# Kernel tuning notes

Hardware: AMD Instinct MI355X
Metric: run time of the kernel (lower is better)

Reference implementation:

```python
import jax, jax.numpy as jnp
import numpy as np

NUM_HEADS = 12
HEAD_DIM = 64  # dim=768 // 12
SCALE = HEAD_DIM ** (-0.5)  # NOTE: original divides q by this -> multiplies by sqrt(head_dim)


def setup_inputs() -> dict:
    key = jax.random.key(0)
    k1, k2, k3 = jax.random.split(key, 3)
    B, N, C = 1, 4096, 768
    x = jax.random.normal(k1, (B, N, C), dtype=jnp.float32)
    qkv_w = jax.random.normal(k2, (3 * C, C), dtype=jnp.float32) * 0.01
    qkv_b = jnp.zeros((3 * C,), dtype=jnp.float32)
    proj_w = jax.random.normal(k3, (C, C), dtype=jnp.float32) * 0.01
    proj_b = jnp.zeros((C,), dtype=jnp.float32)
    return {"x": x, "qkv_w": qkv_w, "qkv_b": qkv_b, "proj_w": proj_w, "proj_b": proj_b}


def reference(x, qkv_w, qkv_b, proj_w, proj_b):
    B, N, C = x.shape
    H, D = NUM_HEADS, HEAD_DIM
    # qkv projection: [B,N,3C]
    qkv = x @ qkv_w.T + qkv_b
    qkv = qkv.reshape(B, N, 3, H, D).transpose(2, 0, 3, 1, 4)  # [3,B,H,N,D]
    q, k, v = qkv[0], qkv[1], qkv[2]
    # Faithful quirk: q / scale with scale = D**-0.5 => logits scaled by sqrt(D)
    attn = jnp.einsum('bhnd,bhmd->bhnm', q / SCALE, k)  # [B,H,N,N]
    attn = jax.nn.softmax(attn, axis=-1)
    # dropout omitted (eval mode / deterministic reference)
    out = jnp.einsum('bhnm,bhmd->bhnd', attn, v)  # [B,H,N,D]
    out = out.transpose(0, 2, 1, 3).reshape(B, N, C)
    out = out @ proj_w.T + proj_b
    return out
```

## Files before the change

kernel.cpp:

```cpp
#include <hip/hip_runtime.h>


typedef short bf16x8 __attribute__((ext_vector_type(8)));
typedef float f32x4 __attribute__((ext_vector_type(4)));
typedef unsigned short u16;
typedef unsigned int u32;

__device__ __forceinline__ u16 f2bf(float f) {
  u32 u = __float_as_uint(f);
  u = (u + 0x7fffu + ((u >> 16) & 1u)) >> 16;
  return (u16)u;
}

__device__ __forceinline__ u32 packbf(float a, float b) {
  u32 ua = __float_as_uint(a), ub = __float_as_uint(b);
  ua += 0x7fffu + ((ua >> 16) & 1u);
  ub += 0x7fffu + ((ub >> 16) & 1u);
  return __builtin_amdgcn_perm(ub, ua, 0x07060302);
}

__device__ __forceinline__ void gload16(const void* g, void* l) {
  __builtin_amdgcn_global_load_lds(
      (const __attribute__((address_space(1))) unsigned int*)g,
      (__attribute__((address_space(3))) unsigned int*)l, 16, 0, 0);
}

__global__ void cast3(const float* __restrict__ a, int na4,
                      const float* __restrict__ b, int nb4,
                      const float* __restrict__ c, int nc4,
                      u16* __restrict__ oa, u16* __restrict__ obp, u16* __restrict__ oc) {
  int i = blockIdx.x * blockDim.x + threadIdx.x;
  const float* src;
  u16* dst;
  int j = i;
  if (i < na4) { src = a; dst = oa; }
  else if (i < na4 + nb4) { src = b; dst = obp; j = i - na4; }
  else if (i < na4 + nb4 + nc4) { src = c; dst = oc; j = i - na4 - nb4; }
  else return;
  float4 v = ((const float4*)src)[j];
  ushort4 o;
  o.x = f2bf(v.x); o.y = f2bf(v.y); o.z = f2bf(v.z); o.w = f2bf(v.w);
  ((ushort4*)dst)[j] = o;
}

template <int MODE>
__global__ __launch_bounds__(256, 2) void gemm_bt(
    const u16* __restrict__ A, const u16* __restrict__ B,
    const float* __restrict__ bias,
    u16* __restrict__ qb, u16* __restrict__ kbuf, u16* __restrict__ vb,
    float* __restrict__ outp, int K, int N) {
  __shared__ __align__(16) u16 As[128 * 32];
  __shared__ __align__(16) u16 Bs[128 * 32];
  const int tid = threadIdx.x, lane = tid & 63, w = tid >> 6;
  const int wr = w >> 1, wc = w & 1, quad = lane >> 4, l15 = lane & 15;
  const int m0 = blockIdx.y * 128, n0 = blockIdx.x * 128;

  f32x4 acc[4][4];
#pragma unroll
  for (int i = 0; i < 4; ++i)
#pragma unroll
    for (int j = 0; j < 4; ++j) acc[i][j] = (f32x4){0.f, 0.f, 0.f, 0.f};

  for (int k0 = 0; k0 < K; k0 += 32) {
    __syncthreads();
#pragma unroll
    for (int i = 0; i < 2; ++i) {
      int chunk = i * 256 + w * 64 + lane;
      int row = chunk >> 2, kc = chunk & 3;
      gload16(A + (size_t)(m0 + row) * K + k0 + kc * 8, (char*)As + chunk * 16);
      gload16(B + (size_t)(n0 + row) * K + k0 + kc * 8, (char*)Bs + chunk * 16);
    }
    __syncthreads();
    bf16x8 af[4], bfr[4];
#pragma unroll
    for (int mi = 0; mi < 4; ++mi)
      af[mi] = *(const bf16x8*)&As[(wr * 64 + mi * 16 + l15) * 32 + quad * 8];
#pragma unroll
    for (int ni = 0; ni < 4; ++ni)
      bfr[ni] = *(const bf16x8*)&Bs[(wc * 64 + ni * 16 + l15) * 32 + quad * 8];
#pragma unroll
    for (int mi = 0; mi < 4; ++mi)
#pragma unroll
      for (int ni = 0; ni < 4; ++ni)
        acc[mi][ni] = __builtin_amdgcn_mfma_f32_16x16x32_bf16(af[mi], bfr[ni], acc[mi][ni], 0, 0, 0);
  }

#pragma unroll
  for (int mi = 0; mi < 4; ++mi) {
    int row = m0 + wr * 64 + mi * 16 + quad * 4;
#pragma unroll
    for (int ni = 0; ni < 4; ++ni) {
      int col = n0 + wc * 64 + ni * 16 + l15;
      float bv = bias[col];
      if (MODE == 0) {
        int t = col / 768;
        int rem = col - t * 768;
        int hh = rem >> 6, d = rem & 63;
        if (t == 2) {
          u16* dst = vb + (size_t)hh * 64 * 4096 + (size_t)d * 4096 + row;
          ushort4 pk;
          pk.x = f2bf(acc[mi][ni][0] + bv);
          pk.y = f2bf(acc[mi][ni][1] + bv);
          pk.z = f2bf(acc[mi][ni][2] + bv);
          pk.w = f2bf(acc[mi][ni][3] + bv);
          *(ushort4*)dst = pk;
        } else {
          u16* dst = (t == 0 ? qb : kbuf) + (size_t)hh * 4096 * 64 + d;
          float sc = (t == 0) ? 11.541560327111707f : 1.f;
#pragma unroll
          for (int r = 0; r < 4; ++r)
            dst[(size_t)(row + r) * 64] = f2bf((acc[mi][ni][r] + bv) * sc);
        }
      } else {
#pragma unroll
        for (int r = 0; r < 4; ++r)
          outp[(size_t)(row + r) * N + col] = acc[mi][ni][r] + bv;
      }
    }
  }
}

__global__ __launch_bounds__(256, 3) void flash_attn(
    const u16* __restrict__ qb, const u16* __restrict__ kb,
    const u16* __restrict__ vtg, u16* __restrict__ ob) {
  constexpr int PLS = 72;
  __shared__ __align__(16) u16 Ks[2][64 * 64];
  __shared__ __align__(16) u16 Vs[2][64 * 64];
  __shared__ __align__(16) u16 pl[4][16 * PLS];

  const int b = blockIdx.x;
  const int g = (b & 7) * 96 + (b >> 3);
  const int h = g >> 6;
  const int q0 = (g & 63) * 64;

  const int tid = threadIdx.x, lane = tid & 63, w = tid >> 6;
  const int quad = lane >> 4, l15 = lane & 15;
  const u16* qh = qb + (size_t)h * 4096 * 64;
  const u16* kh = kb + (size_t)h * 4096 * 64;
  const u16* vh = vtg + (size_t)h * 64 * 4096;
  u16* mypl = &pl[w][0];
  const int sw = l15 & 7;
  const int u0 = (quad ^ sw) * 8;
  const int u1 = ((quad + 4) ^ sw) * 8;

  int c0 = w * 64 + lane, c1 = 256 + w * 64 + lane;
  int r0s = c0 >> 3, j0s = ((c0 & 7) ^ (r0s & 7)) * 8;
  int r1s = c1 >> 3, j1s = ((c1 & 7) ^ (r1s & 7)) * 8;

  bf16x8 qf[2];
#pragma unroll
  for (int c = 0; c < 2; ++c)
    qf[c] = *(const bf16x8*)&qh[(size_t)(q0 + w * 16 + l15) * 64 + c * 32 + quad * 8];

  f32x4 oacc[4];
#pragma unroll
  for (int dt = 0; dt < 4; ++dt) oacc[dt] = (f32x4){0.f, 0.f, 0.f, 0.f};
  float lsum = 0.f;

  gload16(kh + (size_t)r0s * 64 + j0s, (char*)&Ks[0][0] + c0 * 16);
  gload16(kh + (size_t)r1s * 64 + j1s, (char*)&Ks[0][0] + c1 * 16);
  gload16(vh + (size_t)r0s * 4096 + j0s, (char*)&Vs[0][0] + c0 * 16);
  gload16(vh + (size_t)r1s * 4096 + j1s, (char*)&Vs[0][0] + c1 * 16);

  for (int t = 0; t < 64; ++t) {
    const int buf = t & 1;
    __syncthreads();
    if (t < 63) {
      int kt1 = (t + 1) * 64;
      gload16(kh + (size_t)(kt1 + r0s) * 64 + j0s, (char*)&Ks[buf ^ 1][0] + c0 * 16);
      gload16(kh + (size_t)(kt1 + r1s) * 64 + j1s, (char*)&Ks[buf ^ 1][0] + c1 * 16);
      gload16(vh + (size_t)r0s * 4096 + kt1 + j0s, (char*)&Vs[buf ^ 1][0] + c0 * 16);
      gload16(vh + (size_t)r1s * 4096 + kt1 + j1s, (char*)&Vs[buf ^ 1][0] + c1 * 16);
    }

    f32x4 st[4];
#pragma unroll
    for (int nt = 0; nt < 4; ++nt) {
      const u16* kp = &Ks[buf][(nt * 16 + l15) * 64];
      bf16x8 kf0 = *(const bf16x8*)(kp + u0);
      bf16x8 kf1 = *(const bf16x8*)(kp + u1);
      f32x4 z = (f32x4){0.f, 0.f, 0.f, 0.f};
      z = __builtin_amdgcn_mfma_f32_16x16x32_bf16(kf0, qf[0], z, 0, 0, 0);
      st[nt] = __builtin_amdgcn_mfma_f32_16x16x32_bf16(kf1, qf[1], z, 0, 0, 0);
    }

    bf16x8 vf0[4], vf1[4];
#pragma unroll
    for (int dt = 0; dt < 4; ++dt) {
      const u16* vp = &Vs[buf][(dt * 16 + l15) * 64];
      vf0[dt] = *(const bf16x8*)(vp + u0);
      vf1[dt] = *(const bf16x8*)(vp + u1);
    }

    float ls = 0.f;
#pragma unroll
    for (int nt = 0; nt < 4; ++nt) {
      float p0 = __builtin_amdgcn_exp2f(st[nt][0]);
      float p1 = __builtin_amdgcn_exp2f(st[nt][1]);
      float p2 = __builtin_amdgcn_exp2f(st[nt][2]);
      float p3 = __builtin_amdgcn_exp2f(st[nt][3]);
      ls += (p0 + p1) + (p2 + p3);
      uint2 pk;
      pk.x = packbf(p0, p1);
      pk.y = packbf(p2, p3);
      *(uint2*)&mypl[l15 * PLS + nt * 16 + quad * 4] = pk;
    }
    lsum += ls;

    bf16x8 pf0 = *(const bf16x8*)&mypl[l15 * PLS + quad * 8];
    bf16x8 pf1 = *(const bf16x8*)&mypl[l15 * PLS + 32 + quad * 8];
#pragma unroll
    for (int dt = 0; dt < 4; ++dt) {
      oacc[dt] = __builtin_amdgcn_mfma_f32_16x16x32_bf16(pf0, vf0[dt], oacc[dt], 0, 0, 0);
      oacc[dt] = __builtin_amdgcn_mfma_f32_16x16x32_bf16(pf1, vf1[dt], oacc[dt], 0, 0, 0);
    }
  }

  lsum += __shfl_xor(lsum, 16);
  lsum += __shfl_xor(lsum, 32);
  float linv = 1.f / lsum;
  float r0 = __shfl(linv, quad * 4 + 0);
  float r1 = __shfl(linv, quad * 4 + 1);
  float r2 = __shfl(linv, quad * 4 + 2);
  float r3 = __shfl(linv, quad * 4 + 3);
#pragma unroll
  for (int dt = 0; dt < 4; ++dt) {
    int d = dt * 16 + l15;
    int row = q0 + w * 16 + quad * 4;
    u16* op = ob + (size_t)row * 768 + h * 64 + d;
    op[0]       = f2bf(oacc[dt][0] * r0);
    op[768]     = f2bf(oacc[dt][1] * r1);
    op[2 * 768] = f2bf(oacc[dt][2] * r2);
    op[3 * 768] = f2bf(oacc[dt][3] * r3);
  }
}

extern "C" void kernel_launch(void* const* d_in, const int* in_sizes, int n_in,
                              void* d_out, int out_size, void* d_ws, size_t ws_size,
                              hipStream_t stream) {
  const float* x      = (const float*)d_in[0];
  const float* qkv_w  = (const float*)d_in[1];
  const float* qkv_b  = (const float*)d_in[2];
  const float* proj_w = (const float*)d_in[3];
  const float* proj_b = (const float*)d_in[4];
  float* out = (float*)d_out;

  const int N = 4096, C = 768, H = 12, D = 64, C3 = 2304;
  char* ws = (char*)d_ws;
  size_t off = 0;
  u16* xb    = (u16*)(ws + off); off += (size_t)N * C * 2;
  u16* wqkv  = (u16*)(ws + off); off += (size_t)C3 * C * 2;
  u16* wproj = (u16*)(ws + off); off += (size_t)C * C * 2;
  u16* qbuf  = (u16*)(ws + off); off += (size_t)H * N * D * 2;
  u16* kbuf  = (u16*)(ws + off); off += (size_t)H * N * D * 2;
  u16* vbuf  = (u16*)(ws + off); off += (size_t)H * N * D * 2;
  u16* aob = xb;

  const int na4 = N * C / 4, nb4 = C3 * C / 4, nc4 = C * C / 4;
  int ntot = na4 + nb4 + nc4;
  cast3<<<(ntot + 255) / 256, 256, 0, stream>>>(x, na4, qkv_w, nb4, proj_w, nc4, xb, wqkv, wproj);

  dim3 g1(C3 / 128, N / 128);
  gemm_bt<0><<<g1, 256, 0, stream>>>(xb, wqkv, qkv_b, qbuf, kbuf, vbuf, nullptr, C, C3);

  flash_attn<<<768, 256, 0, stream>>>(qbuf, kbuf, vbuf, aob);

  dim3 g3(C / 128, N / 128);
  gemm_bt<1><<<g3, 256, 0, stream>>>(aob, wproj, proj_b, nullptr, nullptr, nullptr, out, C, C);
}
```

Measured before the change: 142.5 us.

## Load K and V fragments directly from global memory, dropping LDS staging

The flash attention kernel no longer stages K and V tiles in double-buffered shared memory via async global-to-LDS loads. Each wave now reads its own MFMA fragments straight from global memory, which removes the per-tile __syncthreads and the LDS traffic. In exchange, the four waves of a block each fetch the same K/V tiles, multiplying global/L2 traffic, and there is no explicit prefetch, so load latency is exposed unless the compiler or occupancy hides it.

Result: slower. 395.2 us (+177.3%).

```diff
diff --git a/kernel.cpp b/kernel.cpp
--- a/kernel.cpp
+++ b/kernel.cpp
@@ -124,8 +124,6 @@
     const u16* __restrict__ qb, const u16* __restrict__ kb,
     const u16* __restrict__ vtg, u16* __restrict__ ob) {
   constexpr int PLS = 72;
-  __shared__ __align__(16) u16 Ks[2][64 * 64];
-  __shared__ __align__(16) u16 Vs[2][64 * 64];
   __shared__ __align__(16) u16 pl[4][16 * PLS];
 
   const int b = blockIdx.x;
@@ -136,16 +134,10 @@
   const int tid = threadIdx.x, lane = tid & 63, w = tid >> 6;
   const int quad = lane >> 4, l15 = lane & 15;
   const u16* qh = qb + (size_t)h * 4096 * 64;
-  const u16* kh = kb + (size_t)h * 4096 * 64;
-  const u16* vh = vtg + (size_t)h * 64 * 4096;
   u16* mypl = &pl[w][0];
-  const int sw = l15 & 7;
-  const int u0 = (quad ^ sw) * 8;
-  const int u1 = ((quad + 4) ^ sw) * 8;
-
-  int c0 = w * 64 + lane, c1 = 256 + w * 64 + lane;
-  int r0s = c0 >> 3, j0s = ((c0 & 7) ^ (r0s & 7)) * 8;
-  int r1s = c1 >> 3, j1s = ((c1 & 7) ^ (r1s & 7)) * 8;
+
+  const u16* kfp = kb + (size_t)h * 4096 * 64 + (size_t)l15 * 64 + quad * 8;
+  const u16* vfp = vtg + (size_t)h * 64 * 4096 + (size_t)l15 * 4096 + quad * 8;
 
   bf16x8 qf[2];
 #pragma unroll
@@ -156,40 +148,29 @@
 #pragma unroll
   for (int dt = 0; dt < 4; ++dt) oacc[dt] = (f32x4){0.f, 0.f, 0.f, 0.f};
   float lsum = 0.f;
-
-  gload16(kh + (size_t)r0s * 64 + j0s, (char*)&Ks[0][0] + c0 * 16);
-  gload16(kh + (size_t)r1s * 64 + j1s, (char*)&Ks[0][0] + c1 * 16);
-  gload16(vh + (size_t)r0s * 4096 + j0s, (char*)&Vs[0][0] + c0 * 16);
-  gload16(vh + (size_t)r1s * 4096 + j1s, (char*)&Vs[0][0] + c1 * 16);
+  const f32x4 zero4 = (f32x4){0.f, 0.f, 0.f, 0.f};
 
   for (int t = 0; t < 64; ++t) {
-    const int buf = t & 1;
-    __syncthreads();
-    if (t < 63) {
-      int kt1 = (t + 1) * 64;
-      gload16(kh + (size_t)(kt1 + r0s) * 64 + j0s, (char*)&Ks[buf ^ 1][0] + c0 * 16);
-      gload16(kh + (size_t)(kt1 + r1s) * 64 + j1s, (char*)&Ks[buf ^ 1][0] + c1 * 16);
-      gload16(vh + (size_t)r0s * 4096 + kt1 + j0s, (char*)&Vs[buf ^ 1][0] + c0 * 16);
-      gload16(vh + (size_t)r1s * 4096 + kt1 + j1s, (char*)&Vs[buf ^ 1][0] + c1 * 16);
+    const u16* kt = kfp + (size_t)t * 64 * 64;
+    bf16x8 kf[4][2];
+#pragma unroll
+    for (int nt = 0; nt < 4; ++nt) {
+      kf[nt][0] = *(const bf16x8*)(kt + nt * 16 * 64);
+      kf[nt][1] = *(const bf16x8*)(kt + nt * 16 * 64 + 32);
+    }
+    const u16* vt = vfp + t * 64;
+    bf16x8 vf0[4], vf1[4];
+#pragma unroll
+    for (int dt = 0; dt < 4; ++dt) {
+      vf0[dt] = *(const bf16x8*)(vt + (size_t)dt * 16 * 4096);
+      vf1[dt] = *(const bf16x8*)(vt + (size_t)dt * 16 * 4096 + 32);
     }
 
     f32x4 st[4];
 #pragma unroll
     for (int nt = 0; nt < 4; ++nt) {
-      const u16* kp = &Ks[buf][(nt * 16 + l15) * 64];
-      bf16x8 kf0 = *(const bf16x8*)(kp + u0);
-      bf16x8 kf1 = *(const bf16x8*)(kp + u1);
-      f32x4 z = (f32x4){0.f, 0.f, 0.f, 0.f};
-      z = __builtin_amdgcn_mfma_f32_16x16x32_bf16(kf0, qf[0], z, 0, 0, 0);
-      st[nt] = __builtin_amdgcn_mfma_f32_16x16x32_bf16(kf1, qf[1], z, 0, 0, 0);
-    }
-
-    bf16x8 vf0[4], vf1[4];
-#pragma unroll
-    for (int dt = 0; dt < 4; ++dt) {
-      const u16* vp = &Vs[buf][(dt * 16 + l15) * 64];
-      vf0[dt] = *(const bf16x8*)(vp + u0);
-      vf1[dt] = *(const bf16x8*)(vp + u1);
+      f32x4 z = __builtin_amdgcn_mfma_f32_16x16x32_bf16(kf[nt][0], qf[0], zero4, 0, 0, 0);
+      st[nt] = __builtin_amdgcn_mfma_f32_16x16x32_bf16(kf[nt][1], qf[1], z, 0, 0, 0);
     }
 
     float ls = 0.f;
```

## Load V fragments directly from global into registers with software prefetch

Applied to the files above, without the earlier changes.

Removes the shared-memory staging of V tiles in the flash attention kernel. Each lane now reads its V-transpose MFMA fragments straight from global memory into registers, prefetching the next tile's fragments one iteration ahead. This drops LDS traffic and halves LDS footprint, which may raise occupancy. In exchange it adds VGPR pressure for the double-buffered fragments and issues uncoalesced-ish 16-byte global loads per lane instead of async LDS copies.

Result: slower. 240.3 us (+68.6%).

```diff
diff --git a/kernel.cpp b/kernel.cpp
--- a/kernel.cpp
+++ b/kernel.cpp
@@ -125,7 +125,6 @@
     const u16* __restrict__ vtg, u16* __restrict__ ob) {
   constexpr int PLS = 72;
   __shared__ __align__(16) u16 Ks[2][64 * 64];
-  __shared__ __align__(16) u16 Vs[2][64 * 64];
   __shared__ __align__(16) u16 pl[4][16 * PLS];
 
   const int b = blockIdx.x;
@@ -137,7 +136,7 @@
   const int quad = lane >> 4, l15 = lane & 15;
   const u16* qh = qb + (size_t)h * 4096 * 64;
   const u16* kh = kb + (size_t)h * 4096 * 64;
-  const u16* vh = vtg + (size_t)h * 64 * 4096;
+  const u16* vfp = vtg + (size_t)h * 64 * 4096 + (size_t)l15 * 4096 + quad * 8;
   u16* mypl = &pl[w][0];
   const int sw = l15 & 7;
   const int u0 = (quad ^ sw) * 8;
@@ -156,11 +155,16 @@
 #pragma unroll
   for (int dt = 0; dt < 4; ++dt) oacc[dt] = (f32x4){0.f, 0.f, 0.f, 0.f};
   float lsum = 0.f;
+  const f32x4 zero4 = (f32x4){0.f, 0.f, 0.f, 0.f};
 
   gload16(kh + (size_t)r0s * 64 + j0s, (char*)&Ks[0][0] + c0 * 16);
   gload16(kh + (size_t)r1s * 64 + j1s, (char*)&Ks[0][0] + c1 * 16);
-  gload16(vh + (size_t)r0s * 4096 + j0s, (char*)&Vs[0][0] + c0 * 16);
-  gload16(vh + (size_t)r1s * 4096 + j1s, (char*)&Vs[0][0] + c1 * 16);
+  bf16x8 vc0[4], vc1[4];
+#pragma unroll
+  for (int dt = 0; dt < 4; ++dt) {
+    vc0[dt] = *(const bf16x8*)(vfp + (size_t)dt * 16 * 4096);
+    vc1[dt] = *(const bf16x8*)(vfp + (size_t)dt * 16 * 4096 + 32);
+  }
 
   for (int t = 0; t < 64; ++t) {
     const int buf = t & 1;
@@ -169,8 +173,13 @@
       int kt1 = (t + 1) * 64;
       gload16(kh + (size_t)(kt1 + r0s) * 64 + j0s, (char*)&Ks[buf ^ 1][0] + c0 * 16);
       gload16(kh + (size_t)(kt1 + r1s) * 64 + j1s, (char*)&Ks[buf ^ 1][0] + c1 * 16);
-      gload16(vh + (size_t)r0s * 4096 + kt1 + j0s, (char*)&Vs[buf ^ 1][0] + c0 * 16);
-      gload16(vh + (size_t)r1s * 4096 + kt1 + j1s, (char*)&Vs[buf ^ 1][0] + c1 * 16);
+    }
+    const int tn = (t < 63) ? t + 1 : 63;
+    bf16x8 vn0[4], vn1[4];
+#pragma unroll
+    for (int dt = 0; dt < 4; ++dt) {
+      vn0[dt] = *(const bf16x8*)(vfp + (size_t)tn * 64 + (size_t)dt * 16 * 4096);
+      vn1[dt] = *(const bf16x8*)(vfp + (size_t)tn * 64 + (size_t)dt * 16 * 4096 + 32);
     }
 
     f32x4 st[4];
@@ -179,17 +188,8 @@
       const u16* kp = &Ks[buf][(nt * 16 + l15) * 64];
       bf16x8 kf0 = *(const bf16x8*)(kp + u0);
       bf16x8 kf1 = *(const bf16x8*)(kp + u1);
-      f32x4 z = (f32x4){0.f, 0.f, 0.f, 0.f};
-      z = __builtin_amdgcn_mfma_f32_16x16x32_bf16(kf0, qf[0], z, 0, 0, 0);
+      f32x4 z = __builtin_amdgcn_mfma_f32_16x16x32_bf16(kf0, qf[0], zero4, 0, 0, 0);
       st[nt] = __builtin_amdgcn_mfma_f32_16x16x32_bf16(kf1, qf[1], z, 0, 0, 0);
-    }
-
-    bf16x8 vf0[4], vf1[4];
-#pragma unroll
-    for (int dt = 0; dt < 4; ++dt) {
-      const u16* vp = &Vs[buf][(dt * 16 + l15) * 64];
-      vf0[dt] = *(const bf16x8*)(vp + u0);
-      vf1[dt] = *(const bf16x8*)(vp + u1);
     }
 
     float ls = 0.f;
@@ -211,9 +211,12 @@
     bf16x8 pf1 = *(const bf16x8*)&mypl[l15 * PLS + 32 + quad * 8];
 #pragma unroll
     for (int dt = 0; dt < 4; ++dt) {
-      oacc[dt] = __builtin_amdgcn_mfma_f32_16x16x32_bf16(pf0, vf0[dt], oacc[dt], 0, 0, 0);
-      oacc[dt] = __builtin_amdgcn_mfma_f32_16x16x32_bf16(pf1, vf1[dt], oacc[dt], 0, 0, 0);
-    }
+      oacc[dt] = __builtin_amdgcn_mfma_f32_16x16x32_bf16(pf0, vc0[dt], oacc[dt], 0, 0, 0);
+      oacc[dt] = __builtin_amdgcn_mfma_f32_16x16x32_bf16(pf1, vc1[dt], oacc[dt], 0, 0, 0);
+    }
+
+#pragma unroll
+    for (int dt = 0; dt < 4; ++dt) { vc0[dt] = vn0[dt]; vc1[dt] = vn1[dt]; }
   }
 
   lsum += __shfl_xor(lsum, 16);
```
